# Performance work log

Measured on AMD Instinct MI355X. Metric: run time of the kernel, lower is better.

Reference implementation:

```python
import jax, jax.numpy as jnp
import numpy as np

DIM = 768
HEADS = 12
DH = DIM // HEADS  # 64
EPS = 1e-5


def layer_norm(x, g, b):
    m = jnp.mean(x, axis=-1, keepdims=True)
    v = jnp.var(x, axis=-1, keepdims=True)
    return (x - m) * jax.lax.rsqrt(v + EPS) * g + b


def setup_inputs() -> dict:
    key = jax.random.key(0)
    ks = jax.random.split(key, 5)
    bs, n = 8, 1025
    x = jax.random.normal(ks[0], (bs, n, DIM), dtype=jnp.float32)
    # torch nn.Linear(dim, 3*dim): store W as [in, out] (already transposed)
    Wqkv = jax.random.normal(ks[1], (DIM, 3 * DIM), dtype=jnp.float32) * 0.02
    bqkv = jnp.zeros((3 * DIM,), dtype=jnp.float32)
    Wproj = jax.random.normal(ks[2], (DIM, DIM), dtype=jnp.float32) * 0.02
    bproj = jnp.zeros((DIM,), dtype=jnp.float32)
    gq = jnp.ones((DH,), dtype=jnp.float32)
    betaq = jnp.zeros((DH,), dtype=jnp.float32)
    gk = jnp.ones((DH,), dtype=jnp.float32)
    betak = jnp.zeros((DH,), dtype=jnp.float32)
    return {"x": x, "Wqkv": Wqkv, "bqkv": bqkv, "Wproj": Wproj,
            "bproj": bproj, "gq": gq, "betaq": betaq, "gk": gk, "betak": betak}


def reference(x, Wqkv, bqkv, Wproj, bproj, gq, betaq, gk, betak):
    bs, n, c = x.shape
    h, dh = HEADS, DH
    qkv = x @ Wqkv + bqkv                      # [bs, n, 3c]
    q, k, v = jnp.split(qkv, 3, axis=-1)
    # [bs, n, c] -> [bs, h, n, dh]
    q = q.reshape(bs, n, h, dh).transpose(0, 2, 1, 3)
    k = k.reshape(bs, n, h, dh).transpose(0, 2, 1, 3)
    v = v.reshape(bs, n, h, dh).transpose(0, 2, 1, 3)
    q = layer_norm(q, gq, betaq)
    k = layer_norm(k, gk, betak)
    score = jnp.einsum('bhnd,bhmd->bhnm', q, k) / np.float32(np.sqrt(dh))
    attn = jax.nn.softmax(score, axis=-1)      # [bs, h, n, n]
    attn_map = attn.mean(axis=1)[:, 0, 1:]     # [bs, n-1]
    out = jnp.einsum('bhnm,bhmd->bhnd', attn, v)
    out = out.transpose(0, 2, 1, 3).reshape(bs, n, c)
    return out @ Wproj + bproj, attn_map
```

## Files before the change

kernel.cpp:

```cpp
#include <hip/hip_runtime.h>
#include <hip/hip_bf16.h>
#include <math.h>

#define BS   8
#define NSEQ 1025
#define DIM  768
#define C3   2304
#define C2   1536
#define HEADS 12
#define DH   64
#define MROWS (BS*NSEQ)
#define MPAD  8320
#define NKPAD 1088
#define QPAD  1152
#define NBH   (BS*HEADS)

#define QSCALE (0.125f * 1.44269504088896340736f)
#define SBOUND 10.0f

typedef __attribute__((ext_vector_type(8))) short bf16x8;
typedef __attribute__((ext_vector_type(4))) float f32x4;

static __device__ __forceinline__ unsigned short f2bf(float f) {
  unsigned int u = __float_as_uint(f);
  unsigned int r = (u + 0x7fffu + ((u >> 16) & 1u)) >> 16;
  return (unsigned short)r;
}

static __device__ __forceinline__ float bf2f(short u) {
  return __uint_as_float(((unsigned int)(unsigned short)u) << 16);
}

static __device__ __forceinline__ unsigned int cvtpk_bf16(float a, float b) {
  unsigned int r;
  asm("v_cvt_pk_bf16_f32 %0, %1, %2" : "=v"(r) : "v"(a), "v"(b));
  return r;
}

static __device__ __forceinline__ void gload16(const short* g, short* l) {
  __builtin_amdgcn_global_load_lds(
      (const __attribute__((address_space(1))) unsigned int*)g,
      (__attribute__((address_space(3))) unsigned int*)l, 16, 0, 0);
}

__global__ __launch_bounds__(256) void convert_x_kernel(
    const float* __restrict__ x, short* __restrict__ xb) {
  const size_t i = ((size_t)blockIdx.x * 256 + threadIdx.x) * 8;
  const size_t row = i / DIM;
  bf16x8 w;
  if (row < MROWS) {
    float4 v0 = *(const float4*)&x[i];
    float4 v1 = *(const float4*)&x[i + 4];
    w[0] = (short)f2bf(v0.x); w[1] = (short)f2bf(v0.y);
    w[2] = (short)f2bf(v0.z); w[3] = (short)f2bf(v0.w);
    w[4] = (short)f2bf(v1.x); w[5] = (short)f2bf(v1.y);
    w[6] = (short)f2bf(v1.z); w[7] = (short)f2bf(v1.w);
  } else {
    #pragma unroll
    for (int j = 0; j < 8; ++j) w[j] = 0;
  }
  *(bf16x8*)&xb[i] = w;
}

__global__ __launch_bounds__(256) void wtrans_kernel(
    const float* __restrict__ W, short* __restrict__ Wt, int K, int N) {
  const int n0 = blockIdx.x * 64, k0 = blockIdx.y * 64;
  __shared__ float tile[64][65];
  const int r = threadIdx.x >> 2;
  const int c0 = (threadIdx.x & 3) * 16;
  const float* src = W + (size_t)(k0 + r) * N + n0 + c0;
  #pragma unroll
  for (int j = 0; j < 16; j += 4) {
    float4 v = *(const float4*)(src + j);
    tile[r][c0 + j]     = v.x;
    tile[r][c0 + j + 1] = v.y;
    tile[r][c0 + j + 2] = v.z;
    tile[r][c0 + j + 3] = v.w;
  }
  __syncthreads();
  bf16x8 w0, w1;
  #pragma unroll
  for (int j = 0; j < 8; ++j) {
    w0[j] = (short)f2bf(tile[c0 + j][r]);
    w1[j] = (short)f2bf(tile[c0 + 8 + j][r]);
  }
  short* dst = Wt + (size_t)(n0 + r) * K + k0 + c0;
  *(bf16x8*)dst = w0;
  *(bf16x8*)(dst + 8) = w1;
}

__global__ __launch_bounds__(256) void gemm_qkv_kernel(
    const short* __restrict__ A, const short* __restrict__ Bt,
    const float* __restrict__ bias, float* __restrict__ qk32,
    short* __restrict__ vb) {
  __shared__ short As[128 * 64];
  __shared__ short Bs[128 * 64];
  const int tid = threadIdx.x;
  const int wid = tid >> 6, lane = tid & 63;
  const int lo = lane & 15, hi = lane >> 4;
  const int wr = wid >> 1, wc = wid & 1;

  const int nwg = gridDim.x * gridDim.y;
  int bid = blockIdx.y * gridDim.x + blockIdx.x;
  {
    const int q = nwg >> 3, rr = nwg & 7;
    const int xcd = bid & 7, idx = bid >> 3;
    bid = (xcd < rr ? xcd * (q + 1) : rr * (q + 1) + (xcd - rr) * q) + idx;
  }
  const int m0 = (bid / gridDim.x) * 128, n0 = (bid % gridDim.x) * 128;

  const int rl = lane >> 3;
  const int cb = (lane & 7) * 8;

  f32x4 acc[4][4];
  #pragma unroll
  for (int m = 0; m < 4; ++m)
    #pragma unroll
    for (int n = 0; n < 4; ++n)
      acc[m][n][0] = acc[m][n][1] = acc[m][n][2] = acc[m][n][3] = 0.f;

  const short* Abase = A + (size_t)(m0 + wid * 32 + rl) * DIM + cb;
  const short* Bbase = Bt + (size_t)(n0 + wid * 32 + rl) * DIM + cb;

  for (int k0 = 0; k0 < DIM; k0 += 64) {
    #pragma unroll
    for (int i = 0; i < 4; ++i) {
      gload16(Abase + (size_t)(i * 8) * DIM + k0, &As[(wid * 32 + i * 8) * 64]);
      gload16(Bbase + (size_t)(i * 8) * DIM + k0, &Bs[(wid * 32 + i * 8) * 64]);
    }
    __syncthreads();
    #pragma unroll
    for (int kk = 0; kk < 2; ++kk) {
      bf16x8 a[4], bfr[4];
      #pragma unroll
      for (int m = 0; m < 4; ++m)
        a[m] = *(const bf16x8*)&As[(wr * 64 + m * 16 + lo) * 64 + kk * 32 + hi * 8];
      #pragma unroll
      for (int n = 0; n < 4; ++n)
        bfr[n] = *(const bf16x8*)&Bs[(wc * 64 + n * 16 + lo) * 64 + kk * 32 + hi * 8];
      #pragma unroll
      for (int m = 0; m < 4; ++m)
        #pragma unroll
        for (int n = 0; n < 4; ++n)
          acc[m][n] = __builtin_amdgcn_mfma_f32_16x16x32_bf16(a[m], bfr[n], acc[m][n], 0, 0, 0);
    }
    __syncthreads();
  }

  const int col0 = n0 + wc * 64;
  const int hglob = col0 >> 6;
  const int htype = hglob / HEADS;
  const int hidx  = hglob - htype * HEADS;
  const float* bp = bias + col0 + lo;

  #pragma unroll
  for (int m = 0; m < 4; ++m) {
    #pragma unroll
    for (int r = 0; r < 4; ++r) {
      const int grow = m0 + wr * 64 + m * 16 + hi * 4 + r;
      if (grow < MROWS) {
        if (htype < 2) {
          float* cp = qk32 + (size_t)grow * C2 + col0 + lo;
          #pragma unroll
          for (int n = 0; n < 4; ++n) cp[n * 16] = acc[m][n][r] + bp[n * 16];
        } else {
          const int brow = grow / NSEQ;
          const int n1 = grow - brow * NSEQ;
          short* dst = vb + ((size_t)(brow * HEADS + hidx) * NKPAD + n1) * DH + lo;
          #pragma unroll
          for (int n = 0; n < 4; ++n)
            dst[n * 16] = (short)f2bf(acc[m][n][r] + bp[n * 16]);
        }
      }
    }
  }
}

__global__ __launch_bounds__(256) void gemm_bf16_kernel(
    const short* __restrict__ A, const short* __restrict__ Bt,
    const float* __restrict__ bias, float* __restrict__ C,
    int M, int N, int K) {
  __shared__ short As[128 * 64];
  __shared__ short Bs[128 * 64];
  const int tid = threadIdx.x;
  const int wid = tid >> 6, lane = tid & 63;
  const int lo = lane & 15, hi = lane >> 4;
  const int wr = wid >> 1, wc = wid & 1;

  const int nwg = gridDim.x * gridDim.y;
  int bid = blockIdx.y * gridDim.x + blockIdx.x;
  {
    const int q = nwg >> 3, rr = nwg & 7;
    const int xcd = bid & 7, idx = bid >> 3;
    bid = (xcd < rr ? xcd * (q + 1) : rr * (q + 1) + (xcd - rr) * q) + idx;
  }
  const int m0 = (bid / gridDim.x) * 128, n0 = (bid % gridDim.x) * 128;

  const int rl = lane >> 3;
  const int cb = (lane & 7) * 8;

  f32x4 acc[4][4];
  #pragma unroll
  for (int m = 0; m < 4; ++m)
    #pragma unroll
    for (int n = 0; n < 4; ++n)
      acc[m][n][0] = acc[m][n][1] = acc[m][n][2] = acc[m][n][3] = 0.f;

  const short* Abase = A + (size_t)(m0 + wid * 32 + rl) * K + cb;
  const short* Bbase = Bt + (size_t)(n0 + wid * 32 + rl) * K + cb;

  for (int k0 = 0; k0 < K; k0 += 64) {
    #pragma unroll
    for (int i = 0; i < 4; ++i) {
      gload16(Abase + (size_t)(i * 8) * K + k0, &As[(wid * 32 + i * 8) * 64]);
      gload16(Bbase + (size_t)(i * 8) * K + k0, &Bs[(wid * 32 + i * 8) * 64]);
    }
    __syncthreads();
    #pragma unroll
    for (int kk = 0; kk < 2; ++kk) {
      bf16x8 a[4], bfr[4];
      #pragma unroll
      for (int m = 0; m < 4; ++m)
        a[m] = *(const bf16x8*)&As[(wr * 64 + m * 16 + lo) * 64 + kk * 32 + hi * 8];
      #pragma unroll
      for (int n = 0; n < 4; ++n)
        bfr[n] = *(const bf16x8*)&Bs[(wc * 64 + n * 16 + lo) * 64 + kk * 32 + hi * 8];
      #pragma unroll
      for (int m = 0; m < 4; ++m)
        #pragma unroll
        for (int n = 0; n < 4; ++n)
          acc[m][n] = __builtin_amdgcn_mfma_f32_16x16x32_bf16(a[m], bfr[n], acc[m][n], 0, 0, 0);
    }
    __syncthreads();
  }

  #pragma unroll
  for (int m = 0; m < 4; ++m) {
    #pragma unroll
    for (int r = 0; r < 4; ++r) {
      const int grow = m0 + wr * 64 + m * 16 + hi * 4 + r;
      if (grow < M) {
        float* cp = C + (size_t)grow * N + n0 + wc * 64 + lo;
        const float* bp = bias + n0 + wc * 64 + lo;
        #pragma unroll
        for (int n = 0; n < 4; ++n) cp[n * 16] = acc[m][n][r] + bp[n * 16];
      }
    }
  }
}

__global__ __launch_bounds__(256) void ln_qk_kernel(
    const float* __restrict__ qk32,
    const float* __restrict__ gq, const float* __restrict__ bq,
    const float* __restrict__ gk, const float* __restrict__ bk,
    short* __restrict__ qb, short* __restrict__ kb) {
  const int task = blockIdx.x * 4 + (threadIdx.x >> 6);
  const int lane = threadIdx.x & 63;
  const int TASKS = MROWS * HEADS;
  if (task >= TASKS) return;
  const int row = task / HEADS;
  const int h = task - row * HEADS;
  const size_t base = (size_t)row * C2 + h * DH;
  float xq = qk32[base + lane];
  float xk = qk32[base + DIM + lane];
  float sq = xq, s2q = xq * xq, sk = xk, s2k = xk * xk;
  #pragma unroll
  for (int off = 32; off; off >>= 1) {
    sq  += __shfl_xor(sq,  off);
    s2q += __shfl_xor(s2q, off);
    sk  += __shfl_xor(sk,  off);
    s2k += __shfl_xor(s2k, off);
  }
  const float inv64 = 1.f / 64.f;
  float mq = sq * inv64, vq = s2q * inv64 - mq * mq;
  float mk = sk * inv64, vk = s2k * inv64 - mk * mk;
  float rq = rsqrtf(vq + 1e-5f), rk = rsqrtf(vk + 1e-5f);
  float qn = ((xq - mq) * rq * gq[lane] + bq[lane]) * QSCALE;
  float kn =  (xk - mk) * rk * gk[lane] + bk[lane];
  const int b = row / NSEQ;
  const int n = row - b * NSEQ;
  const int bh = b * HEADS + h;
  qb[((size_t)bh * QPAD  + n) * DH + lane] = (short)f2bf(qn);
  kb[((size_t)bh * NKPAD + n) * DH + lane] = (short)f2bf(kn);
}

__global__ __launch_bounds__(256) void vt_convert_kernel(
    const short* __restrict__ vb, short* __restrict__ vt) {
  const int kt = blockIdx.x;
  const int bh = blockIdx.y;
  const int t = threadIdx.x;
  __shared__ float tile[64][65];
  const int r = t >> 2;
  const int c0 = (t & 3) * 16;
  const int grow = kt * 64 + r;

  if (grow < NSEQ) {
    const short* src = vb + ((size_t)bh * NKPAD + grow) * DH + c0;
    bf16x8 a = *(const bf16x8*)src;
    bf16x8 b2 = *(const bf16x8*)(src + 8);
    #pragma unroll
    for (int j = 0; j < 8; ++j) {
      tile[r][c0 + j]     = bf2f(a[j]);
      tile[r][c0 + 8 + j] = bf2f(b2[j]);
    }
  } else {
    #pragma unroll
    for (int j = 0; j < 16; ++j) tile[r][c0 + j] = 0.f;
  }
  __syncthreads();
  bf16x8 w0, w1;
  #pragma unroll
  for (int j = 0; j < 8; ++j) {
    w0[j] = (short)f2bf(tile[c0 + j][r]);
    w1[j] = (short)f2bf(tile[c0 + 8 + j][r]);
  }
  short* dst = vt + ((size_t)bh * DH + r) * NKPAD + kt * 64 + c0;
  *(bf16x8*)dst = w0;
  *(bf16x8*)(dst + 8) = w1;
}

__global__ __launch_bounds__(256) void attn_mfma_kernel(
    const short* __restrict__ qb, const short* __restrict__ kb,
    const short* __restrict__ vt, short* __restrict__ ab) {
  const int bh = blockIdx.x;
  const int b = bh / HEADS, h = bh - (bh / HEADS) * HEADS;
  const int wid = threadIdx.x >> 6;
  const int lane = threadIdx.x & 63;
  const int lo = lane & 15, hi = lane >> 4;
  const int q0 = blockIdx.y * 128;
  const int xsw = (lo & 7) << 3;

  __shared__ short Ks[64 * 64];
  __shared__ short Vs[64 * 64];
  __shared__ short Pb[4][32][72];

  const short* kg = kb + (size_t)bh * NKPAD * DH;
  const short* vg = vt + (size_t)bh * DH * NKPAD;

  const int sr = wid * 16 + (lane >> 3);
  const int sw = ((lane & 7) ^ (lane >> 3)) << 3;
  auto stageK = [&](int kt) {
    #pragma unroll
    for (int i = 0; i < 2; ++i)
      gload16(kg + (size_t)(kt * 64 + sr + i * 8) * DH + sw,
              &Ks[wid * 1024 + i * 512]);
  };
  auto stageV = [&](int kt) {
    #pragma unroll
    for (int i = 0; i < 2; ++i)
      gload16(vg + (size_t)(sr + i * 8) * NKPAD + kt * 64 + sw,
              &Vs[wid * 1024 + i * 512]);
  };

  bf16x8 aq[2][2];
  #pragma unroll
  for (int m = 0; m < 2; ++m) {
    const short* qp = qb + (size_t)bh * QPAD * DH
                    + (size_t)(q0 + wid * 32 + m * 16 + lo) * DH + hi * 8;
    aq[m][0] = *(const bf16x8*)qp;
    aq[m][1] = *(const bf16x8*)(qp + 32);
  }

  f32x4 o[2][4];
  float lsum[2][4];
  #pragma unroll
  for (int m = 0; m < 2; ++m)
    #pragma unroll
    for (int nt = 0; nt < 4; ++nt) {
      o[m][nt][0] = o[m][nt][1] = o[m][nt][2] = o[m][nt][3] = 0.f;
      lsum[m][nt] = 0.f;
    }

  stageK(0);
  stageV(0);
  __syncthreads();

  for (int kt = 0; kt < 17; ++kt) {
    f32x4 s[2][4];
    #pragma unroll
    for (int m = 0; m < 2; ++m)
      #pragma unroll
      for (int nt = 0; nt < 4; ++nt)
        s[m][nt][0] = s[m][nt][1] = s[m][nt][2] = s[m][nt][3] = 0.f;
    __builtin_amdgcn_s_setprio(1);
    #pragma unroll
    for (int kk = 0; kk < 2; ++kk) {
      bf16x8 kf[4];
      #pragma unroll
      for (int nt = 0; nt < 4; ++nt)
        kf[nt] = *(const bf16x8*)&Ks[(nt * 16 + lo) * 64
                                     + ((kk * 32 + hi * 8) ^ xsw)];
      #pragma unroll
      for (int m = 0; m < 2; ++m)
        #pragma unroll
        for (int nt = 0; nt < 4; ++nt)
          s[m][nt] = __builtin_amdgcn_mfma_f32_16x16x32_bf16(
              aq[m][kk], kf[nt], s[m][nt], 0, 0, 0);
    }
    __builtin_amdgcn_s_setprio(0);

    __syncthreads();
    if (kt < 16) stageK(kt + 1);

    if (kt == 16) {
      #pragma unroll
      for (int m = 0; m < 2; ++m)
        #pragma unroll
        for (int nt = 0; nt < 4; ++nt)
          if (nt * 16 + lo >= 1)
            s[m][nt][0] = s[m][nt][1] = s[m][nt][2] = s[m][nt][3] = -1e30f;
    }
    #pragma unroll
    for (int m = 0; m < 2; ++m)
      #pragma unroll
      for (int nt = 0; nt < 4; ++nt) {
        float p0 = exp2f(s[m][nt][0] - SBOUND);
        float p1 = exp2f(s[m][nt][1] - SBOUND);
        float p2 = exp2f(s[m][nt][2] - SBOUND);
        float p3 = exp2f(s[m][nt][3] - SBOUND);
        lsum[m][0] += p0; lsum[m][1] += p1;
        lsum[m][2] += p2; lsum[m][3] += p3;
        unsigned int c01 = cvtpk_bf16(p0, p1);
        unsigned int c23 = cvtpk_bf16(p2, p3);
        unsigned short* pb = (unsigned short*)&Pb[wid][m * 16 + 4 * hi][nt * 16 + lo];
        pb[0]       = (unsigned short)c01;
        pb[72]      = (unsigned short)(c01 >> 16);
        pb[144]     = (unsigned short)c23;
        pb[216]     = (unsigned short)(c23 >> 16);
      }
    __builtin_amdgcn_s_setprio(1);
    #pragma unroll
    for (int ks = 0; ks < 2; ++ks) {
      bf16x8 pa0 = *(const bf16x8*)&Pb[wid][lo][ks * 32 + hi * 8];
      bf16x8 pa1 = *(const bf16x8*)&Pb[wid][16 + lo][ks * 32 + hi * 8];
      #pragma unroll
      for (int nt = 0; nt < 4; ++nt) {
        bf16x8 vf = *(const bf16x8*)&Vs[(nt * 16 + lo) * 64
                                        + ((ks * 32 + hi * 8) ^ xsw)];
        o[0][nt] = __builtin_amdgcn_mfma_f32_16x16x32_bf16(pa0, vf, o[0][nt], 0, 0, 0);
        o[1][nt] = __builtin_amdgcn_mfma_f32_16x16x32_bf16(pa1, vf, o[1][nt], 0, 0, 0);
      }
    }
    __builtin_amdgcn_s_setprio(0);

    __syncthreads();
    if (kt < 16) stageV(kt + 1);
  }

  #pragma unroll
  for (int m = 0; m < 2; ++m)
    #pragma unroll
    for (int r = 0; r < 4; ++r) {
      float v = lsum[m][r];
      v += __shfl_xor(v, 1);
      v += __shfl_xor(v, 2);
      v += __shfl_xor(v, 4);
      v += __shfl_xor(v, 8);
      lsum[m][r] = v;
    }
  #pragma unroll
  for (int m = 0; m < 2; ++m)
    #pragma unroll
    for (int r = 0; r < 4; ++r) {
      const int qrow = q0 + wid * 32 + m * 16 + 4 * hi + r;
      if (qrow < NSEQ) {
        const float inv = 1.f / lsum[m][r];
        short* op = ab + (size_t)(b * NSEQ + qrow) * DIM + h * DH + lo;
        #pragma unroll
        for (int nt = 0; nt < 4; ++nt)
          op[nt * 16] = (short)f2bf(o[m][nt][r] * inv);
      }
    }
}

__global__ __launch_bounds__(256) void map_ms_kernel(
    const short* __restrict__ qb, const short* __restrict__ kb,
    float* __restrict__ ms) {
  const int bh = blockIdx.x;
  const int tid = threadIdx.x;
  __shared__ float q0s[64];
  __shared__ float red[256];
  if (tid < 64) q0s[tid] = bf2f(qb[(size_t)bh * QPAD * DH + tid]);
  __syncthreads();
  float s[5];
  float lm = -INFINITY;
  #pragma unroll
  for (int sl = 0; sl < 5; ++sl) {
    int j = tid + sl * 256;
    s[sl] = -INFINITY;
    if (j < NSEQ) {
      const short* kp = kb + ((size_t)bh * NKPAD + j) * DH;
      float d0 = 0.f;
      #pragma unroll
      for (int c = 0; c < 8; ++c) {
        bf16x8 kv = *(const bf16x8*)(kp + c * 8);
        #pragma unroll
        for (int e = 0; e < 8; ++e) d0 += q0s[c * 8 + e] * bf2f(kv[e]);
      }
      s[sl] = d0;
      lm = fmaxf(lm, d0);
    }
  }
  red[tid] = lm; __syncthreads();
  for (int off = 128; off > 0; off >>= 1) {
    if (tid < off) red[tid] = fmaxf(red[tid], red[tid + off]);
    __syncthreads();
  }
  const float Mx = red[0]; __syncthreads();
  float ls = 0.f;
  #pragma unroll
  for (int sl = 0; sl < 5; ++sl) {
    int j = tid + sl * 256;
    if (j < NSEQ) ls += exp2f(s[sl] - Mx);
  }
  red[tid] = ls; __syncthreads();
  for (int off = 128; off > 0; off >>= 1) {
    if (tid < off) red[tid] += red[tid + off];
    __syncthreads();
  }
  if (tid == 0) {
    ms[bh * 2]     = Mx;
    ms[bh * 2 + 1] = 1.f / (red[0] * (float)HEADS);
  }
}

__global__ __launch_bounds__(256) void map_p_kernel(
    const short* __restrict__ qb, const short* __restrict__ kb,
    const float* __restrict__ ms, float* __restrict__ map) {
  const int b = blockIdx.y;
  const int j = blockIdx.x * 256 + threadIdx.x + 1;
  const int tid = threadIdx.x;
  __shared__ float q0s[768];
  __shared__ float msb[24];
  for (int idx = tid; idx < 768; idx += 256) {
    const int h = idx >> 6, d = idx & 63;
    q0s[idx] = bf2f(qb[(size_t)(b * HEADS + h) * QPAD * DH + d]);
  }
  if (tid < 24) msb[tid] = ms[b * HEADS * 2 + tid];
  __syncthreads();
  float acc = 0.f;
  #pragma unroll
  for (int h = 0; h < HEADS; ++h) {
    const short* kp = kb + ((size_t)(b * HEADS + h) * NKPAD + j) * DH;
    float d0 = 0.f;
    #pragma unroll
    for (int c = 0; c < 8; ++c) {
      bf16x8 kv = *(const bf16x8*)(kp + c * 8);
      const float* qp = &q0s[h * DH + c * 8];
      #pragma unroll
      for (int e = 0; e < 8; ++e) d0 += qp[e] * bf2f(kv[e]);
    }
    acc += exp2f(d0 - msb[h * 2]) * msb[h * 2 + 1];
  }
  map[(size_t)b * (NSEQ - 1) + j - 1] = acc;
}

extern "C" void kernel_launch(void* const* d_in, const int* in_sizes, int n_in,
                              void* d_out, int out_size, void* d_ws, size_t ws_size,
                              hipStream_t stream) {
  const float* x     = (const float*)d_in[0];
  const float* Wqkv  = (const float*)d_in[1];
  const float* bqkv  = (const float*)d_in[2];
  const float* Wproj = (const float*)d_in[3];
  const float* bproj = (const float*)d_in[4];
  const float* gq    = (const float*)d_in[5];
  const float* betaq = (const float*)d_in[6];
  const float* gk    = (const float*)d_in[7];
  const float* betak = (const float*)d_in[8];

  float* qk32 = (float*)d_ws;
  short* xb  = (short*)(qk32 + (size_t)MROWS * C2);
  short* qb  = xb + (size_t)MPAD * DIM;
  short* kb  = qb + (size_t)NBH * QPAD * DH;
  short* vb  = kb + (size_t)NBH * NKPAD * DH;
  short* vt  = vb + (size_t)NBH * NKPAD * DH;
  short* wqt = vt + (size_t)NBH * DH * NKPAD;
  short* wpt = wqt + (size_t)C3 * DIM;
  float* ms  = (float*)(wpt + (size_t)DIM * DIM);
  float* out = (float*)d_out;
  float* map = out + (size_t)MROWS * DIM;

  convert_x_kernel<<<MPAD * DIM / 2048, 256, 0, stream>>>(x, xb);
  {
    dim3 grid(C3 / 64, DIM / 64);
    wtrans_kernel<<<grid, 256, 0, stream>>>(Wqkv, wqt, DIM, C3);
  }
  {
    dim3 grid(DIM / 64, DIM / 64);
    wtrans_kernel<<<grid, 256, 0, stream>>>(Wproj, wpt, DIM, DIM);
  }
  {
    dim3 grid(C3 / 128, MPAD / 128);
    gemm_qkv_kernel<<<grid, 256, 0, stream>>>(xb, wqt, bqkv, qk32, vb);
  }
  {
    int blocks = (MROWS * HEADS + 3) / 4;
    ln_qk_kernel<<<blocks, 256, 0, stream>>>(qk32, gq, betaq, gk, betak, qb, kb);
  }
  {
    dim3 grid(17, NBH);
    vt_convert_kernel<<<grid, 256, 0, stream>>>(vb, vt);
  }
  {
    dim3 grid(NBH, QPAD / 128);
    attn_mfma_kernel<<<grid, 256, 0, stream>>>(qb, kb, vt, xb);
  }
  map_ms_kernel<<<NBH, 256, 0, stream>>>(qb, kb, ms);
  {
    dim3 grid(4, BS);
    map_p_kernel<<<grid, 256, 0, stream>>>(qb, kb, ms, map);
  }
  {
    dim3 grid(DIM / 128, MPAD / 128);
    gemm_bf16_kernel<<<grid, 256, 0, stream>>>(xb, wpt, bproj, out, MROWS, DIM, DIM);
  }
}
```

Before: 229.7 us.

## Fuse Q/K LayerNorm into QKV GEMM epilogue and drop fp32 intermediate

The per-head LayerNorm for Q and K now runs inside the QKV GEMM epilogue. Each wave reduces its 64-column head slice with shuffles within 16 lanes and writes normalized bf16 Q and K directly. This removes the separate ln_qk kernel launch and the large fp32 qk32 buffer round trip through global memory. The row padding MPAD is also raised, which adds one extra row of GEMM tiles of padded work.

```diff
diff --git a/kernel.cpp b/kernel.cpp
--- a/kernel.cpp
+++ b/kernel.cpp
@@ -6,11 +6,10 @@
 #define NSEQ 1025
 #define DIM  768
 #define C3   2304
-#define C2   1536
 #define HEADS 12
 #define DH   64
 #define MROWS (BS*NSEQ)
-#define MPAD  8320
+#define MPAD  8448
 #define NKPAD 1088
 #define QPAD  1152
 #define NBH   (BS*HEADS)
@@ -91,8 +90,10 @@
 
 __global__ __launch_bounds__(256) void gemm_qkv_kernel(
     const short* __restrict__ A, const short* __restrict__ Bt,
-    const float* __restrict__ bias, float* __restrict__ qk32,
-    short* __restrict__ vb) {
+    const float* __restrict__ bias,
+    const float* __restrict__ gq, const float* __restrict__ bq,
+    const float* __restrict__ gk, const float* __restrict__ bk,
+    short* __restrict__ qb, short* __restrict__ kb, short* __restrict__ vb) {
   __shared__ short As[128 * 64];
   __shared__ short Bs[128 * 64];
   const int tid = threadIdx.x;
@@ -153,23 +154,62 @@
   const int hidx  = hglob - htype * HEADS;
   const float* bp = bias + col0 + lo;
 
+  float gl[4], bl[4];
+  if (htype == 0) {
+    #pragma unroll
+    for (int nt = 0; nt < 4; ++nt) { gl[nt] = gq[nt * 16 + lo]; bl[nt] = bq[nt * 16 + lo]; }
+  } else if (htype == 1) {
+    #pragma unroll
+    for (int nt = 0; nt < 4; ++nt) { gl[nt] = gk[nt * 16 + lo]; bl[nt] = bk[nt * 16 + lo]; }
+  }
+
   #pragma unroll
   for (int m = 0; m < 4; ++m) {
     #pragma unroll
     for (int r = 0; r < 4; ++r) {
       const int grow = m0 + wr * 64 + m * 16 + hi * 4 + r;
       if (grow < MROWS) {
-        if (htype < 2) {
-          float* cp = qk32 + (size_t)grow * C2 + col0 + lo;
+        const int brow = grow / NSEQ;
+        const int n1 = grow - brow * NSEQ;
+        const int bh = brow * HEADS + hidx;
+        float v[4];
+        #pragma unroll
+        for (int nt = 0; nt < 4; ++nt) v[nt] = acc[m][nt][r] + bp[nt * 16];
+        if (htype == 2) {
+          short* dst = vb + ((size_t)bh * NKPAD + n1) * DH + lo;
           #pragma unroll
-          for (int n = 0; n < 4; ++n) cp[n * 16] = acc[m][n][r] + bp[n * 16];
+          for (int nt = 0; nt < 4; ++nt) dst[nt * 16] = (short)f2bf(v[nt]);
         } else {
-          const int brow = grow / NSEQ;
-          const int n1 = grow - brow * NSEQ;
-          short* dst = vb + ((size_t)(brow * HEADS + hidx) * NKPAD + n1) * DH + lo;
+          float s2v[4];
           #pragma unroll
-          for (int n = 0; n < 4; ++n)
-            dst[n * 16] = (short)f2bf(acc[m][n][r] + bp[n * 16]);
+          for (int nt = 0; nt < 4; ++nt) s2v[nt] = v[nt] * v[nt];
+          float t[4], t2[4];
+          #pragma unroll
+          for (int nt = 0; nt < 4; ++nt) {
+            t[nt]  = v[nt]   + v[nt ^ 2];
+            t2[nt] = s2v[nt] + s2v[nt ^ 2];
+          }
+          float u  = t[0]  + t[1];
+          float u2 = t2[0] + t2[1];
+          u  += __shfl_xor(u,  8);  u2 += __shfl_xor(u2, 8);
+          u  += __shfl_xor(u,  4);  u2 += __shfl_xor(u2, 4);
+          u  += __shfl_xor(u,  2);  u2 += __shfl_xor(u2, 2);
+          u  += __shfl_xor(u,  1);  u2 += __shfl_xor(u2, 1);
+          const float inv64 = 1.f / 64.f;
+          const float mean = u * inv64;
+          const float var  = u2 * inv64 - mean * mean;
+          const float rr = rsqrtf(var + 1e-5f);
+          if (htype == 0) {
+            short* dst = qb + ((size_t)bh * QPAD + n1) * DH + lo;
+            #pragma unroll
+            for (int nt = 0; nt < 4; ++nt)
+              dst[nt * 16] = (short)f2bf(((v[nt] - mean) * rr * gl[nt] + bl[nt]) * QSCALE);
+          } else {
+            short* dst = kb + ((size_t)bh * NKPAD + n1) * DH + lo;
+            #pragma unroll
+            for (int nt = 0; nt < 4; ++nt)
+              dst[nt * 16] = (short)f2bf((v[nt] - mean) * rr * gl[nt] + bl[nt]);
+          }
         }
       }
     }
@@ -247,41 +287,6 @@
       }
     }
   }
-}
-
-__global__ __launch_bounds__(256) void ln_qk_kernel(
-    const float* __restrict__ qk32,
-    const float* __restrict__ gq, const float* __restrict__ bq,
-    const float* __restrict__ gk, const float* __restrict__ bk,
-    short* __restrict__ qb, short* __restrict__ kb) {
-  const int task = blockIdx.x * 4 + (threadIdx.x >> 6);
-  const int lane = threadIdx.x & 63;
-  const int TASKS = MROWS * HEADS;
-  if (task >= TASKS) return;
-  const int row = task / HEADS;
-  const int h = task - row * HEADS;
-  const size_t base = (size_t)row * C2 + h * DH;
-  float xq = qk32[base + lane];
-  float xk = qk32[base + DIM + lane];
-  float sq = xq, s2q = xq * xq, sk = xk, s2k = xk * xk;
-  #pragma unroll
-  for (int off = 32; off; off >>= 1) {
-    sq  += __shfl_xor(sq,  off);
-    s2q += __shfl_xor(s2q, off);
-    sk  += __shfl_xor(sk,  off);
-    s2k += __shfl_xor(s2k, off);
-  }
-  const float inv64 = 1.f / 64.f;
-  float mq = sq * inv64, vq = s2q * inv64 - mq * mq;
-  float mk = sk * inv64, vk = s2k * inv64 - mk * mk;
-  float rq = rsqrtf(vq + 1e-5f), rk = rsqrtf(vk + 1e-5f);
-  float qn = ((xq - mq) * rq * gq[lane] + bq[lane]) * QSCALE;
-  float kn =  (xk - mk) * rk * gk[lane] + bk[lane];
-  const int b = row / NSEQ;
-  const int n = row - b * NSEQ;
-  const int bh = b * HEADS + h;
-  qb[((size_t)bh * QPAD  + n) * DH + lane] = (short)f2bf(qn);
-  kb[((size_t)bh * NKPAD + n) * DH + lane] = (short)f2bf(kn);
 }
 
 __global__ __launch_bounds__(256) void vt_convert_kernel(
@@ -568,8 +573,7 @@
   const float* gk    = (const float*)d_in[7];
   const float* betak = (const float*)d_in[8];
 
-  float* qk32 = (float*)d_ws;
-  short* xb  = (short*)(qk32 + (size_t)MROWS * C2);
+  short* xb  = (short*)d_ws;
   short* qb  = xb + (size_t)MPAD * DIM;
   short* kb  = qb + (size_t)NBH * QPAD * DH;
   short* vb  = kb + (size_t)NBH * NKPAD * DH;
@@ -591,11 +595,8 @@
   }
   {
     dim3 grid(C3 / 128, MPAD / 128);
-    gemm_qkv_kernel<<<grid, 256, 0, stream>>>(xb, wqt, bqkv, qk32, vb);
-  }
-  {
-    int blocks = (MROWS * HEADS + 3) / 4;
-    ln_qk_kernel<<<blocks, 256, 0, stream>>>(qk32, gq, betaq, gk, betak, qb, kb);
+    gemm_qkv_kernel<<<grid, 256, 0, stream>>>(xb, wqt, bqkv,
+                                              gq, betaq, gk, betak, qb, kb, vb);
   }
   {
     dim3 grid(17, NBH);
```

After: 213.2 us. 7.2% less time.
